# Performance work log

Hardware: AMD Instinct MI355X
Metric: run time of the kernel (lower is better)

Reference implementation:

```python
import jax, jax.numpy as jnp
import numpy as np

K = 128      # classes
CIN = 128    # ch_in
CL = 128     # ch_latent
B, H, W = 8, 1, 8192
SLOPE = 0.01 # F.leaky_relu default
EPS = 1e-5   # BatchNorm eps


def lrelu(x):
    return jnp.where(x >= 0, x, SLOPE * x)


def conv1x1(x, w, b):
    # x: (B,C,H,W), w: (O,C), b: (O,)
    return jnp.einsum('bchw,oc->bohw', x, w) + b[None, :, None, None]


def bn_eval(x, gamma, beta, mean, var):
    scale = gamma * jax.lax.rsqrt(var + EPS)
    return x * scale[None, :, None, None] + (beta - mean * scale)[None, :, None, None]


def setup_inputs() -> dict:
    key = jax.random.key(0)
    ks = jax.random.split(key, 16)
    def w(k, shape, fan_in):
        return jax.random.normal(k, shape, jnp.float32) / np.sqrt(fan_in)
    return {
        'x_in': jax.random.normal(ks[0], (B, CIN, H, W), jnp.float32),
        'cl1_w': w(ks[1], (CL, CIN), CIN), 'cl1_b': jnp.zeros((CL,), jnp.float32),
        'bn1_gamma': jnp.ones((CL,), jnp.float32), 'bn1_beta': jnp.zeros((CL,), jnp.float32),
        'bn1_mean': 0.1 * jax.random.normal(ks[2], (CL,), jnp.float32),
        'bn1_var': jax.random.uniform(ks[3], (CL,), jnp.float32, 0.5, 1.5),
        'cl2_w': w(ks[4], (CL, CL), CL), 'cl2_b': jnp.zeros((CL,), jnp.float32),
        'cl3_w': w(ks[5], (K + 1, CL), CL), 'cl3_b': jnp.zeros((K + 1,), jnp.float32),
        'reg1_w': w(ks[6], (CL, CIN), CIN), 'reg1_b': jnp.zeros((CL,), jnp.float32),
        'bnr_gamma': jnp.ones((CL,), jnp.float32), 'bnr_beta': jnp.zeros((CL,), jnp.float32),
        'bnr_mean': 0.1 * jax.random.normal(ks[7], (CL,), jnp.float32),
        'bnr_var': jax.random.uniform(ks[8], (CL,), jnp.float32, 0.5, 1.5),
        'cm2_w': w(ks[9], (K, CL, 32), CL), 'cm2_b': jnp.zeros((K, 32), jnp.float32),
        'cm3_w': w(ks[10], (K, 32, 1), 32), 'cm3_b': jnp.zeros((K, 1), jnp.float32),
    }


def reference(x_in, cl1_w, cl1_b, bn1_gamma, bn1_beta, bn1_mean, bn1_var,
              cl2_w, cl2_b, cl3_w, cl3_b,
              reg1_w, reg1_b, bnr_gamma, bnr_beta, bnr_mean, bnr_var,
              cm2_w, cm2_b, cm3_w, cm3_b):
    # classification branch
    x = lrelu(bn_eval(conv1x1(x_in, cl1_w, cl1_b), bn1_gamma, bn1_beta, bn1_mean, bn1_var))
    x = lrelu(conv1x1(x, cl2_w, cl2_b))
    x = conv1x1(x, cl3_w, cl3_b)                    # (B, K+1, H, W)
    logits = x[:, :K]
    mask = lrelu(x[:, -1:])                          # (B,1,H,W)
    inds = jnp.argmax(logits, axis=1)                # (B,H,W) int
    inds_r = inds.reshape(-1).astype(jnp.int32)      # (N,)
    xr = lrelu(bn_eval(conv1x1(x_in, reg1_w, reg1_b), bnr_gamma, bnr_beta, bnr_mean, bnr_var))
    # torch: transpose(1,3).reshape(-1, C)  -> (B,W,H,C) flatten
    xr = jnp.transpose(xr, (0, 3, 2, 1)).reshape(-1, CL)   # (N, CL)
    # CondMul 1: per-pixel gathered weight (N,CL,32)
    h = lrelu(jnp.einsum('ni,nio->no', xr, cm2_w[inds_r]) + cm2_b[inds_r])
    # CondMul 2: (N,32)->(N,1)
    reg = jnp.einsum('ni,nio->no', h, cm3_w[inds_r]) + cm3_b[inds_r]
    reg = reg.reshape(B, 1, 1, -1)                   # (B,1,1,H*W)
    x_real = (inds[:, None].astype(jnp.float32) + reg) * (1.0 / K)
    return x_real, mask
```

## Files before the change

kernel.cpp:

```cpp
#include <hip/hip_runtime.h>
#include <math.h>

#define NPOS 65536
#define NCH  128
#define DELTA 0.008f

#define OFF_XR   0u
#define OFF_W1T  8388608u
#define OFF_W2T  (OFF_W1T + 16384u)
#define OFF_W3T  (OFF_W2T + 16384u)
#define OFF_B1F  (OFF_W3T + 16384u)
#define OFF_BRF  (OFF_B1F + 128u)
#define OFF_B2F  (OFF_BRF + 128u)
#define OFF_B3F  (OFF_B2F + 128u)
#define OFF_BF16 (OFF_B3F + 132u)
#define OFF_INT  (OFF_BF16 + 329728u)

#define UW1H 0u
#define UW1L 16384u
#define UWRH 32768u
#define UWRL 49152u
#define UW2H 65536u
#define UW2L 81920u
#define UW3H 98304u
#define UW3L 116736u
#define UW2K 135168u

#define NST 2080

typedef short bf16x8 __attribute__((ext_vector_type(8)));
typedef float f32x4 __attribute__((ext_vector_type(4)));
#define MFMA16 __builtin_amdgcn_mfma_f32_16x16x32_bf16

__device__ __forceinline__ float lrelu(float v) { return v >= 0.0f ? v : 0.01f * v; }
__device__ __forceinline__ unsigned short f2bf(float f) {
    unsigned u = __float_as_uint(f);
    return (unsigned short)((u + 0x7fffu + ((u >> 16) & 1u)) >> 16);
}
__device__ __forceinline__ float bf2f(unsigned short h) {
    return __uint_as_float(((unsigned)h) << 16);
}
__device__ __forceinline__ unsigned long long pack4(unsigned short a, unsigned short b,
                                                    unsigned short c, unsigned short d) {
    return (unsigned long long)a | ((unsigned long long)b << 16)
         | ((unsigned long long)c << 32) | ((unsigned long long)d << 48);
}

__global__ void k_prep(const float* __restrict__ cl1_w, const float* __restrict__ cl1_b,
                       const float* __restrict__ g1, const float* __restrict__ be1,
                       const float* __restrict__ mu1, const float* __restrict__ va1,
                       const float* __restrict__ cl2_w, const float* __restrict__ cl2_b,
                       const float* __restrict__ cl3_w, const float* __restrict__ cl3_b,
                       const float* __restrict__ reg1_w, const float* __restrict__ reg1_b,
                       const float* __restrict__ gr, const float* __restrict__ ber,
                       const float* __restrict__ mur, const float* __restrict__ var_,
                       const float* __restrict__ cm2w,
                       float* __restrict__ ws_f, unsigned short* __restrict__ wbf,
                       int* __restrict__ hist, int* __restrict__ fixcnt)
{
    const int bid = blockIdx.x;
    const int t = threadIdx.x;
    if (bid >= 128) {
        __shared__ float tl[32 * 132];
        int k = bid - 128;
        #pragma unroll
        for (int i = 0; i < 32; ++i) {
            float v = cm2w[(unsigned)k * 4096u + i * 128 + t];
            int ci = i * 4 + (t >> 5), o = t & 31;
            tl[o * 132 + ci] = v;
        }
        __syncthreads();
        #pragma unroll
        for (int i = 0; i < 32; ++i)
            wbf[UW2K + (unsigned)k * 4096u + i * 128 + t] = f2bf(tl[i * 132 + t]);
        return;
    }
    int tid = bid * 128 + t;
    int cin = tid >> 7, cout = tid & 127;
    float s1 = g1[cout] / sqrtf(va1[cout] + 1e-5f);
    float sr = gr[cout] / sqrtf(var_[cout] + 1e-5f);
    float w1 = cl1_w[cout * 128 + cin] * s1;
    float wr = reg1_w[cout * 128 + cin] * sr;
    float w2 = cl2_w[cout * 128 + cin];
    float w3 = cl3_w[cout * 128 + cin];
    ws_f[OFF_W1T + tid] = w1;
    ws_f[OFF_W2T + tid] = w2;
    ws_f[OFF_W3T + tid] = w3;
    int j = cout * 128 + cin;
    unsigned short h;
    h = f2bf(w1); wbf[UW1H + j] = h; wbf[UW1L + j] = f2bf(w1 - bf2f(h));
    h = f2bf(wr); wbf[UWRH + j] = h; wbf[UWRL + j] = f2bf(wr - bf2f(h));
    h = f2bf(w2); wbf[UW2H + j] = h; wbf[UW2L + j] = f2bf(w2 - bf2f(h));
    h = f2bf(w3); wbf[UW3H + j] = h; wbf[UW3L + j] = f2bf(w3 - bf2f(h));
    if (tid < 2048) {
        int r = tid >> 7, ci = tid & 127;
        float v = (r == 0) ? cl3_w[128 * 128 + ci] : 0.0f;
        int jj = (128 + r) * 128 + ci;
        h = f2bf(v); wbf[UW3H + jj] = h; wbf[UW3L + jj] = f2bf(v - bf2f(h));
    }
    if (tid < 128) {
        float s1b = g1[tid] / sqrtf(va1[tid] + 1e-5f);
        float srb = gr[tid] / sqrtf(var_[tid] + 1e-5f);
        ws_f[OFF_B1F + tid] = cl1_b[tid] * s1b + be1[tid] - mu1[tid] * s1b;
        ws_f[OFF_BRF + tid] = reg1_b[tid] * srb + ber[tid] - mur[tid] * srb;
        ws_f[OFF_B2F + tid] = cl2_b[tid];
        hist[tid] = 0;
    }
    if (tid < 129) ws_f[OFF_B3F + tid] = cl3_b[tid];
    if (tid == 0) fixcnt[0] = 0;
}

__global__ __launch_bounds__(256, 2)
void k_fused(const float* __restrict__ X, const float* __restrict__ wsf,
             const unsigned short* __restrict__ wbf,
             float* __restrict__ XR, float* __restrict__ out_mask,
             int* __restrict__ inds, int* __restrict__ fixcnt,
             int* __restrict__ fixlist)
{
    __shared__ __align__(16) unsigned short XBh[64 * 136];
    __shared__ __align__(16) unsigned short XBl[64 * 136];
    __shared__ float sm1[4 * 64];
    __shared__ float sm2[4 * 64];
    __shared__ int   si1[4 * 64];

    const int t = threadIdx.x;
    const int lane = t & 63;
    const int cl16 = lane & 15;
    const int q8 = (lane >> 4) * 8;
    const int q4 = (lane >> 4) * 4;
    const int wv = __builtin_amdgcn_readfirstlane(t >> 6);
    const unsigned nt64 = blockIdx.x * 64u;
    const unsigned base = nt64 + (nt64 >> 13) * 1040384u;

    const unsigned short* W1H = wbf + UW1H; const unsigned short* W1L = wbf + UW1L;
    const unsigned short* WRH = wbf + UWRH; const unsigned short* WRL = wbf + UWRL;
    const unsigned short* W2H = wbf + UW2H; const unsigned short* W2L = wbf + UW2L;
    const unsigned short* W3H = wbf + UW3H; const unsigned short* W3L = wbf + UW3L;
    const float* b1f = wsf + OFF_B1F;
    const float* brf = wsf + OFF_BRF;
    const float* b2f = wsf + OFF_B2F;
    const float* b3f = wsf + OFF_B3F;

    const f32x4 vzero = {0.f, 0.f, 0.f, 0.f};

    {
        const int pos = t & 63, cig = t >> 6;
        #pragma unroll
        for (int l = 0; l < 8; ++l) {
            int ci0 = cig * 32 + l * 4;
            float v0 = X[base + (unsigned)(ci0 + 0) * 8192u + pos];
            float v1 = X[base + (unsigned)(ci0 + 1) * 8192u + pos];
            float v2 = X[base + (unsigned)(ci0 + 2) * 8192u + pos];
            float v3 = X[base + (unsigned)(ci0 + 3) * 8192u + pos];
            unsigned short h0 = f2bf(v0), h1 = f2bf(v1), h2 = f2bf(v2), h3 = f2bf(v3);
            unsigned long long ph = pack4(h0, h1, h2, h3);
            unsigned long long pl = pack4(f2bf(v0 - bf2f(h0)), f2bf(v1 - bf2f(h1)),
                                          f2bf(v2 - bf2f(h2)), f2bf(v3 - bf2f(h3)));
            *(unsigned long long*)&XBh[pos * 136 + ci0] = ph;
            *(unsigned long long*)&XBl[pos * 136 + ci0] = pl;
        }
    }
    __syncthreads();

    f32x4 aY[2][4], aR[2][4];
    #pragma unroll
    for (int m = 0; m < 2; ++m)
        #pragma unroll
        for (int n = 0; n < 4; ++n) { aY[m][n] = vzero; aR[m][n] = vzero; }
    #pragma unroll
    for (int kt = 0; kt < 4; ++kt) {
        bf16x8 Bh[4], Bl[4];
        #pragma unroll
        for (int n = 0; n < 4; ++n) {
            int bo = (n * 16 + cl16) * 136 + kt * 32 + q8;
            Bh[n] = *(const bf16x8*)&XBh[bo];
            Bl[n] = *(const bf16x8*)&XBl[bo];
        }
        #pragma unroll
        for (int m = 0; m < 2; ++m) {
            int ao = (wv * 32 + m * 16 + cl16) * 128 + kt * 32 + q8;
            bf16x8 a1h = *(const bf16x8*)&W1H[ao], a1l = *(const bf16x8*)&W1L[ao];
            bf16x8 arh = *(const bf16x8*)&WRH[ao], arl = *(const bf16x8*)&WRL[ao];
            #pragma unroll
            for (int n = 0; n < 4; ++n) {
                aY[m][n] = MFMA16(a1h, Bl[n], aY[m][n], 0, 0, 0);
                aY[m][n] = MFMA16(a1l, Bh[n], aY[m][n], 0, 0, 0);
                aY[m][n] = MFMA16(a1h, Bh[n], aY[m][n], 0, 0, 0);
                aR[m][n] = MFMA16(arh, Bl[n], aR[m][n], 0, 0, 0);
                aR[m][n] = MFMA16(arl, Bh[n], aR[m][n], 0, 0, 0);
                aR[m][n] = MFMA16(arh, Bh[n], aR[m][n], 0, 0, 0);
            }
        }
    }
    __syncthreads();

    {
        #pragma unroll
        for (int m = 0; m < 2; ++m) {
            int cb = wv * 32 + m * 16 + q4;
            float br0 = brf[cb], br1 = brf[cb + 1], br2 = brf[cb + 2], br3 = brf[cb + 3];
            #pragma unroll
            for (int n = 0; n < 4; ++n) {
                unsigned pb = (nt64 + n * 16 + cl16) * 128u + cb;
                XR[pb]     = lrelu(aR[m][n][0] + br0);
                XR[pb + 1] = lrelu(aR[m][n][1] + br1);
                XR[pb + 2] = lrelu(aR[m][n][2] + br2);
                XR[pb + 3] = lrelu(aR[m][n][3] + br3);
            }
        }
    }
    {
        #pragma unroll
        for (int m = 0; m < 2; ++m) {
            int cb = wv * 32 + m * 16 + q4;
            float b0 = b1f[cb], b1 = b1f[cb + 1], b2 = b1f[cb + 2], b3 = b1f[cb + 3];
            #pragma unroll
            for (int n = 0; n < 4; ++n) {
                float v0 = lrelu(aY[m][n][0] + b0), v1 = lrelu(aY[m][n][1] + b1);
                float v2 = lrelu(aY[m][n][2] + b2), v3 = lrelu(aY[m][n][3] + b3);
                unsigned short h0 = f2bf(v0), h1 = f2bf(v1), h2 = f2bf(v2), h3 = f2bf(v3);
                unsigned long long ph = pack4(h0, h1, h2, h3);
                unsigned long long pl = pack4(f2bf(v0 - bf2f(h0)), f2bf(v1 - bf2f(h1)),
                                              f2bf(v2 - bf2f(h2)), f2bf(v3 - bf2f(h3)));
                int idx = (n * 16 + cl16) * 136 + cb;
                *(unsigned long long*)&XBh[idx] = ph;
                *(unsigned long long*)&XBl[idx] = pl;
            }
        }
    }
    __syncthreads();

    f32x4 aZ[2][4];
    #pragma unroll
    for (int m = 0; m < 2; ++m)
        #pragma unroll
        for (int n = 0; n < 4; ++n) aZ[m][n] = vzero;
    #pragma unroll
    for (int kt = 0; kt < 4; ++kt) {
        bf16x8 Bh[4], Bl[4];
        #pragma unroll
        for (int n = 0; n < 4; ++n) {
            int bo = (n * 16 + cl16) * 136 + kt * 32 + q8;
            Bh[n] = *(const bf16x8*)&XBh[bo];
            Bl[n] = *(const bf16x8*)&XBl[bo];
        }
        #pragma unroll
        for (int m = 0; m < 2; ++m) {
            int ao = (wv * 32 + m * 16 + cl16) * 128 + kt * 32 + q8;
            bf16x8 ah = *(const bf16x8*)&W2H[ao], al = *(const bf16x8*)&W2L[ao];
            #pragma unroll
            for (int n = 0; n < 4; ++n) {
                aZ[m][n] = MFMA16(ah, Bl[n], aZ[m][n], 0, 0, 0);
                aZ[m][n] = MFMA16(al, Bh[n], aZ[m][n], 0, 0, 0);
                aZ[m][n] = MFMA16(ah, Bh[n], aZ[m][n], 0, 0, 0);
            }
        }
    }
    __syncthreads();
    {
        #pragma unroll
        for (int m = 0; m < 2; ++m) {
            int cb = wv * 32 + m * 16 + q4;
            float b0 = b2f[cb], b1 = b2f[cb + 1], b2 = b2f[cb + 2], b3 = b2f[cb + 3];
            #pragma unroll
            for (int n = 0; n < 4; ++n) {
                float v0 = lrelu(aZ[m][n][0] + b0), v1 = lrelu(aZ[m][n][1] + b1);
                float v2 = lrelu(aZ[m][n][2] + b2), v3 = lrelu(aZ[m][n][3] + b3);
                unsigned short h0 = f2bf(v0), h1 = f2bf(v1), h2 = f2bf(v2), h3 = f2bf(v3);
                unsigned long long ph = pack4(h0, h1, h2, h3);
                unsigned long long pl = pack4(f2bf(v0 - bf2f(h0)), f2bf(v1 - bf2f(h1)),
                                              f2bf(v2 - bf2f(h2)), f2bf(v3 - bf2f(h3)));
                int idx = (n * 16 + cl16) * 136 + cb;
                *(unsigned long long*)&XBh[idx] = ph;
                *(unsigned long long*)&XBl[idx] = pl;
            }
        }
    }
    __syncthreads();

    f32x4 aL[2][4], aM[4];
    #pragma unroll
    for (int m = 0; m < 2; ++m)
        #pragma unroll
        for (int n = 0; n < 4; ++n) aL[m][n] = vzero;
    #pragma unroll
    for (int n = 0; n < 4; ++n) aM[n] = vzero;
    #pragma unroll
    for (int kt = 0; kt < 4; ++kt) {
        bf16x8 Bh[4], Bl[4];
        #pragma unroll
        for (int n = 0; n < 4; ++n) {
            int bo = (n * 16 + cl16) * 136 + kt * 32 + q8;
            Bh[n] = *(const bf16x8*)&XBh[bo];
            Bl[n] = *(const bf16x8*)&XBl[bo];
        }
        #pragma unroll
        for (int m = 0; m < 2; ++m) {
            int ao = (wv * 32 + m * 16 + cl16) * 128 + kt * 32 + q8;
            bf16x8 ah = *(const bf16x8*)&W3H[ao], al = *(const bf16x8*)&W3L[ao];
            #pragma unroll
            for (int n = 0; n < 4; ++n) {
                aL[m][n] = MFMA16(ah, Bl[n], aL[m][n], 0, 0, 0);
                aL[m][n] = MFMA16(al, Bh[n], aL[m][n], 0, 0, 0);
                aL[m][n] = MFMA16(ah, Bh[n], aL[m][n], 0, 0, 0);
            }
        }
        if (wv == 3) {
            int ao = (128 + cl16) * 128 + kt * 32 + q8;
            bf16x8 ah = *(const bf16x8*)&W3H[ao], al = *(const bf16x8*)&W3L[ao];
            #pragma unroll
            for (int n = 0; n < 4; ++n) {
                aM[n] = MFMA16(ah, Bl[n], aM[n], 0, 0, 0);
                aM[n] = MFMA16(al, Bh[n], aM[n], 0, 0, 0);
                aM[n] = MFMA16(ah, Bh[n], aM[n], 0, 0, 0);
            }
        }
    }

    {
        float bb[2][4];
        #pragma unroll
        for (int m = 0; m < 2; ++m) {
            int cb = wv * 32 + m * 16 + q4;
            bb[m][0] = b3f[cb]; bb[m][1] = b3f[cb + 1];
            bb[m][2] = b3f[cb + 2]; bb[m][3] = b3f[cb + 3];
        }
        float m1[4], m2[4]; int i1[4];
        #pragma unroll
        for (int n = 0; n < 4; ++n) {
            m1[n] = -1e30f; m2[n] = -1e30f; i1[n] = 0;
            #pragma unroll
            for (int m = 0; m < 2; ++m) {
                int cb = wv * 32 + m * 16 + q4;
                #pragma unroll
                for (int r = 0; r < 4; ++r) {
                    float v = aL[m][n][r] + bb[m][r];
                    if (v > m1[n]) { m2[n] = m1[n]; m1[n] = v; i1[n] = cb + r; }
                    else if (v > m2[n]) m2[n] = v;
                }
            }
        }
        #pragma unroll
        for (int off = 16; off <= 32; off <<= 1) {
            #pragma unroll
            for (int n = 0; n < 4; ++n) {
                float om1 = __shfl_xor(m1[n], off);
                float om2 = __shfl_xor(m2[n], off);
                int   oi1 = __shfl_xor(i1[n], off);
                if (om1 > m1[n] || (om1 == m1[n] && oi1 < i1[n])) {
                    m2[n] = fmaxf(m1[n], om2); m1[n] = om1; i1[n] = oi1;
                } else {
                    m2[n] = fmaxf(m2[n], om1);
                }
            }
        }
        if ((lane >> 4) == 0) {
            #pragma unroll
            for (int n = 0; n < 4; ++n) {
                sm1[wv * 64 + n * 16 + cl16] = m1[n];
                sm2[wv * 64 + n * 16 + cl16] = m2[n];
                si1[wv * 64 + n * 16 + cl16] = i1[n];
            }
        }
    }
    if (wv == 3 && (lane >> 4) == 0) {
        float mb = b3f[128];
        #pragma unroll
        for (int n = 0; n < 4; ++n)
            out_mask[nt64 + n * 16 + cl16] = lrelu(aM[n][0] + mb);
    }
    __syncthreads();
    if (t < 64) {
        float m1 = sm1[t], m2 = sm2[t];
        int i1 = si1[t];
        #pragma unroll
        for (int w = 1; w < 4; ++w) {
            float v1 = sm1[w * 64 + t];
            float v2 = sm2[w * 64 + t];
            int   vi = si1[w * 64 + t];
            if (v1 > m1) { m2 = fmaxf(m1, v2); m1 = v1; i1 = vi; }
            else         { m2 = fmaxf(m2, v1); }
        }
        int n = nt64 + t;
        inds[n] = i1;
        if (m1 - m2 < DELTA) {
            int slot = atomicAdd(fixcnt, 1);
            fixlist[slot] = n;
        }
    }
}

__global__ __launch_bounds__(256, 4)
void k_fix(const float* __restrict__ X, const float* __restrict__ wsf,
           const int* __restrict__ fixcnt, const int* __restrict__ fixlist,
           int* __restrict__ inds)
{
    const int cnt = fixcnt[0];
    const int t = threadIdx.x;
    const int lane = t & 63;
    const int wv = t >> 6;
    const float* W1T = wsf + OFF_W1T;
    const float* W2T = wsf + OFF_W2T;
    const float* W3T = wsf + OFF_W3T;
    const float* b1f = wsf + OFF_B1F;
    const float* b2f = wsf + OFF_B2F;
    const float* b3f = wsf + OFF_B3F;

    for (int idx = blockIdx.x * 4 + wv; idx < cnt; idx += 1024) {
        int n = fixlist[idx];
        const float* xb = X + (unsigned)(n >> 13) * 1048576u + (unsigned)(n & 8191);
        float x0 = xb[(unsigned)lane * 8192u];
        float x1 = xb[(unsigned)(64 + lane) * 8192u];
        float a0, a1;
        a0 = 0.f; a1 = 0.f;
        for (int ci = 0; ci < 64; ++ci) {
            float xv = __shfl(x0, ci);
            const float* wr = W1T + ci * 128;
            a0 = fmaf(wr[lane], xv, a0);
            a1 = fmaf(wr[64 + lane], xv, a1);
        }
        for (int ci = 0; ci < 64; ++ci) {
            float xv = __shfl(x1, ci);
            const float* wr = W1T + (64 + ci) * 128;
            a0 = fmaf(wr[lane], xv, a0);
            a1 = fmaf(wr[64 + lane], xv, a1);
        }
        x0 = lrelu(a0 + b1f[lane]); x1 = lrelu(a1 + b1f[64 + lane]);
        a0 = 0.f; a1 = 0.f;
        for (int ci = 0; ci < 64; ++ci) {
            float xv = __shfl(x0, ci);
            const float* wr = W2T + ci * 128;
            a0 = fmaf(wr[lane], xv, a0);
            a1 = fmaf(wr[64 + lane], xv, a1);
        }
        for (int ci = 0; ci < 64; ++ci) {
            float xv = __shfl(x1, ci);
            const float* wr = W2T + (64 + ci) * 128;
            a0 = fmaf(wr[lane], xv, a0);
            a1 = fmaf(wr[64 + lane], xv, a1);
        }
        x0 = lrelu(a0 + b2f[lane]); x1 = lrelu(a1 + b2f[64 + lane]);
        a0 = 0.f; a1 = 0.f;
        for (int ci = 0; ci < 64; ++ci) {
            float xv = __shfl(x0, ci);
            const float* wr = W3T + ci * 128;
            a0 = fmaf(wr[lane], xv, a0);
            a1 = fmaf(wr[64 + lane], xv, a1);
        }
        for (int ci = 0; ci < 64; ++ci) {
            float xv = __shfl(x1, ci);
            const float* wr = W3T + (64 + ci) * 128;
            a0 = fmaf(wr[lane], xv, a0);
            a1 = fmaf(wr[64 + lane], xv, a1);
        }
        float L0 = a0 + b3f[lane], L1 = a1 + b3f[64 + lane];
        float v; int id;
        if (L0 >= L1) { v = L0; id = lane; } else { v = L1; id = 64 + lane; }
        #pragma unroll
        for (int off = 1; off < 64; off <<= 1) {
            float ov = __shfl_xor(v, off);
            int   oi = __shfl_xor(id, off);
            if (ov > v || (ov == v && oi < id)) { v = ov; id = oi; }
        }
        if (lane == 0) inds[n] = id;
    }
}

__global__ void k_hist(const int* __restrict__ inds, int* __restrict__ hist)
{
    __shared__ int lh[128];
    int t = threadIdx.x;
    if (t < 128) lh[t] = 0;
    __syncthreads();
    atomicAdd(&lh[inds[blockIdx.x * 256 + t]], 1);
    __syncthreads();
    if (t < 128 && lh[t] > 0) atomicAdd(&hist[t], lh[t]);
}

__global__ void k_scan(const int* __restrict__ hist, int* __restrict__ off,
                       int* __restrict__ cur, int* __restrict__ tiles,
                       int* __restrict__ ntt)
{
    __shared__ int s[128];
    __shared__ int s2[128];
    int t = threadIdx.x;
    int v = hist[t];
    int ntk = (v + 127) >> 7;
    s[t] = v;
    s2[t] = ntk;
    __syncthreads();
    for (int d = 1; d < 128; d <<= 1) {
        int a  = (t >= d) ? s[t - d]  : 0;
        int a2 = (t >= d) ? s2[t - d] : 0;
        __syncthreads();
        s[t] += a;
        s2[t] += a2;
        __syncthreads();
    }
    off[t] = s[t] - v;
    cur[t] = s[t] - v;
    int tb = s2[t] - ntk;
    for (int j = 0; j < ntk; ++j)
        tiles[tb + j] = (t << 16) | j;
    if (t == 127) ntt[0] = s2[127];
}

__global__ void k_scatter(const int* __restrict__ inds, int* __restrict__ cur,
                          int* __restrict__ bucket)
{
    __shared__ int lh[128];
    __shared__ int gb[128];
    int t = threadIdx.x;
    if (t < 128) lh[t] = 0;
    __syncthreads();
    int n = blockIdx.x * 256 + t;
    int id = inds[n];
    int r = atomicAdd(&lh[id], 1);
    __syncthreads();
    if (t < 128 && lh[t] > 0) gb[t] = atomicAdd(&cur[t], lh[t]);
    __syncthreads();
    bucket[gb[id] + r] = n;
}

__global__ __launch_bounds__(256, 4)
void k_reg(const float* __restrict__ XR, const unsigned short* __restrict__ wbf,
           const float* __restrict__ cm2b, const float* __restrict__ cm3w,
           const float* __restrict__ cm3b, const int* __restrict__ hist,
           const int* __restrict__ off, const int* __restrict__ bucket,
           const int* __restrict__ tiles, const int* __restrict__ ntt,
           float* __restrict__ out)
{
    __shared__ __align__(16) unsigned short XP[8 * NST];
    __shared__ float red[128];
    int bid = blockIdx.x;
    if (bid >= ntt[0]) return;
    int desc = tiles[bid];
    int k = desc >> 16;
    int start = (desc & 0xffff) << 7;
    int cnt = hist[k];
    int base = off[k];
    int t = threadIdx.x;
    int lane = t & 63;
    int wv = __builtin_amdgcn_readfirstlane(t >> 6);
    const int n16 = lane & 15;
    const int quad = lane >> 4;

    #pragma unroll
    for (int half = 0; half < 2; ++half) {
        int rs = (t >> 2) + half * 64;
        int q = t & 3;
        int sidx = start + rs;
        if (sidx >= cnt) sidx = cnt - 1;
        int n = bucket[base + sidx];
        const float4* src = (const float4*)(XR + (unsigned)n * 128u + q * 32);
        unsigned db = (rs >> 4) * NST + q * 512 + (rs & 15) * 8;
        #pragma unroll
        for (int qg = 0; qg < 4; ++qg) {
            float4 fa = src[qg * 2], fb = src[qg * 2 + 1];
            unsigned long long pa = pack4(f2bf(fa.x), f2bf(fa.y), f2bf(fa.z), f2bf(fa.w));
            unsigned long long pb = pack4(f2bf(fb.x), f2bf(fb.y), f2bf(fb.z), f2bf(fb.w));
            *(unsigned long long*)&XP[db + qg * 128]     = pa;
            *(unsigned long long*)&XP[db + qg * 128 + 4] = pb;
        }
    }
    __syncthreads();

    const unsigned short* wb = wbf + UW2K + (unsigned)k * 4096u;
    bf16x8 Bf[2][4];
    #pragma unroll
    for (int nf = 0; nf < 2; ++nf)
        #pragma unroll
        for (int kt = 0; kt < 4; ++kt)
            Bf[nf][kt] = *(const bf16x8*)&wb[(nf * 16 + n16) * 128 + kt * 32 + quad * 8];

    const f32x4 vzero = {0.f, 0.f, 0.f, 0.f};
    f32x4 acc[2][2];
    acc[0][0] = vzero; acc[0][1] = vzero; acc[1][0] = vzero; acc[1][1] = vzero;
    #pragma unroll
    for (int kt = 0; kt < 4; ++kt) {
        bf16x8 Af[2];
        #pragma unroll
        for (int mf = 0; mf < 2; ++mf)
            Af[mf] = *(const bf16x8*)&XP[(wv * 2 + mf) * NST + kt * 512 + lane * 8];
        #pragma unroll
        for (int mf = 0; mf < 2; ++mf)
            #pragma unroll
            for (int nf = 0; nf < 2; ++nf)
                acc[mf][nf] = MFMA16(Af[mf], Bf[nf][kt], acc[mf][nf], 0, 0, 0);
    }

    float b2a = cm2b[k * 32 + n16], b2b = cm2b[k * 32 + 16 + n16];
    float w3a = cm3w[k * 32 + n16], w3b = cm3w[k * 32 + 16 + n16];
    const int m0 = wv * 32;
    #pragma unroll
    for (int mf = 0; mf < 2; ++mf) {
        #pragma unroll
        for (int r = 0; r < 4; ++r) {
            float p = lrelu(acc[mf][0][r] + b2a) * w3a
                    + lrelu(acc[mf][1][r] + b2b) * w3b;
            p += __shfl_xor(p, 1);
            p += __shfl_xor(p, 2);
            p += __shfl_xor(p, 4);
            p += __shfl_xor(p, 8);
            if (n16 == 0)
                red[m0 + mf * 16 + quad * 4 + r] = p;
        }
    }
    __syncthreads();
    if (t < 128 && start + t < cnt) {
        int n2 = bucket[base + start + t];
        out[n2] = ((float)k + red[t] + cm3b[k]) * (1.0f / 128.0f);
    }
}

extern "C" void kernel_launch(void* const* d_in, const int* in_sizes, int n_in,
                              void* d_out, int out_size, void* d_ws, size_t ws_size,
                              hipStream_t stream)
{
    (void)in_sizes; (void)n_in; (void)out_size; (void)ws_size;
    const float* x_in   = (const float*)d_in[0];
    const float* cl1_w  = (const float*)d_in[1];
    const float* cl1_b  = (const float*)d_in[2];
    const float* g1     = (const float*)d_in[3];
    const float* be1    = (const float*)d_in[4];
    const float* mu1    = (const float*)d_in[5];
    const float* va1    = (const float*)d_in[6];
    const float* cl2_w  = (const float*)d_in[7];
    const float* cl2_b  = (const float*)d_in[8];
    const float* cl3_w  = (const float*)d_in[9];
    const float* cl3_b  = (const float*)d_in[10];
    const float* reg1_w = (const float*)d_in[11];
    const float* reg1_b = (const float*)d_in[12];
    const float* gr     = (const float*)d_in[13];
    const float* ber    = (const float*)d_in[14];
    const float* mur    = (const float*)d_in[15];
    const float* var_   = (const float*)d_in[16];
    const float* cm2w   = (const float*)d_in[17];
    const float* cm2b   = (const float*)d_in[18];
    const float* cm3w   = (const float*)d_in[19];
    const float* cm3b   = (const float*)d_in[20];

    float* ws_f = (float*)d_ws;
    float* XR   = ws_f + OFF_XR;
    unsigned short* wbf = (unsigned short*)(ws_f + OFF_BF16);
    int*   wsi    = (int*)(ws_f + OFF_INT);
    int*   inds   = wsi;
    int*   hist   = inds + 65536;
    int*   offb   = hist + 128;
    int*   cur    = offb + 128;
    int*   ntt    = cur + 128;
    int*   fixcnt = ntt + 4;
    int*   tiles  = fixcnt + 4;
    int*   fixlist= tiles + 1024;
    int*   bucket = fixlist + 65536;
    float* out = (float*)d_out;

    hipLaunchKernelGGL(k_prep, dim3(256), dim3(128), 0, stream,
                       cl1_w, cl1_b, g1, be1, mu1, va1, cl2_w, cl2_b, cl3_w, cl3_b,
                       reg1_w, reg1_b, gr, ber, mur, var_, cm2w, ws_f, wbf, hist, fixcnt);
    hipLaunchKernelGGL(k_fused, dim3(1024), dim3(256), 0, stream,
                       x_in, ws_f, wbf, XR, out + 65536, inds, fixcnt, fixlist);
    hipLaunchKernelGGL(k_fix, dim3(256), dim3(256), 0, stream,
                       x_in, ws_f, fixcnt, fixlist, inds);
    hipLaunchKernelGGL(k_hist, dim3(256), dim3(256), 0, stream, inds, hist);
    hipLaunchKernelGGL(k_scan, dim3(1), dim3(128), 0, stream,
                       hist, offb, cur, tiles, ntt);
    hipLaunchKernelGGL(k_scatter, dim3(256), dim3(256), 0, stream, inds, cur, bucket);
    hipLaunchKernelGGL(k_reg, dim3(768), dim3(256), 0, stream,
                       XR, wbf, cm2b, cm3w, cm3b, hist, offb, bucket, tiles, ntt, out);
}
```

Baseline: 244.7 us.

## Store regression latent as bf16, fold histogram into fused kernel, halve reg tiles

```diff
diff --git a/kernel.cpp b/kernel.cpp
--- a/kernel.cpp
+++ b/kernel.cpp
@@ -113,9 +113,9 @@
 __global__ __launch_bounds__(256, 2)
 void k_fused(const float* __restrict__ X, const float* __restrict__ wsf,
              const unsigned short* __restrict__ wbf,
-             float* __restrict__ XR, float* __restrict__ out_mask,
-             int* __restrict__ inds, int* __restrict__ fixcnt,
-             int* __restrict__ fixlist)
+             unsigned short* __restrict__ XRB, float* __restrict__ out_mask,
+             int* __restrict__ inds, int* __restrict__ hist,
+             int* __restrict__ fixcnt, int* __restrict__ fixlist)
 {
     __shared__ __align__(16) unsigned short XBh[64 * 136];
     __shared__ __align__(16) unsigned short XBl[64 * 136];
@@ -202,10 +202,12 @@
             #pragma unroll
             for (int n = 0; n < 4; ++n) {
                 unsigned pb = (nt64 + n * 16 + cl16) * 128u + cb;
-                XR[pb]     = lrelu(aR[m][n][0] + br0);
-                XR[pb + 1] = lrelu(aR[m][n][1] + br1);
-                XR[pb + 2] = lrelu(aR[m][n][2] + br2);
-                XR[pb + 3] = lrelu(aR[m][n][3] + br3);
+                ushort4 xo;
+                xo.x = f2bf(lrelu(aR[m][n][0] + br0));
+                xo.y = f2bf(lrelu(aR[m][n][1] + br1));
+                xo.z = f2bf(lrelu(aR[m][n][2] + br2));
+                xo.w = f2bf(lrelu(aR[m][n][3] + br3));
+                *(ushort4*)&XRB[pb] = xo;
             }
         }
     }
@@ -383,6 +385,7 @@
         }
         int n = nt64 + t;
         inds[n] = i1;
+        atomicAdd(&hist[i1], 1);
         if (m1 - m2 < DELTA) {
             int slot = atomicAdd(fixcnt, 1);
             fixlist[slot] = n;
@@ -393,7 +396,7 @@
 __global__ __launch_bounds__(256, 4)
 void k_fix(const float* __restrict__ X, const float* __restrict__ wsf,
            const int* __restrict__ fixcnt, const int* __restrict__ fixlist,
-           int* __restrict__ inds)
+           int* __restrict__ inds, int* __restrict__ hist)
 {
     const int cnt = fixcnt[0];
     const int t = threadIdx.x;
@@ -462,19 +465,15 @@
             int   oi = __shfl_xor(id, off);
             if (ov > v || (ov == v && oi < id)) { v = ov; id = oi; }
         }
-        if (lane == 0) inds[n] = id;
-    }
-}
-
-__global__ void k_hist(const int* __restrict__ inds, int* __restrict__ hist)
-{
-    __shared__ int lh[128];
-    int t = threadIdx.x;
-    if (t < 128) lh[t] = 0;
-    __syncthreads();
-    atomicAdd(&lh[inds[blockIdx.x * 256 + t]], 1);
-    __syncthreads();
-    if (t < 128 && lh[t] > 0) atomicAdd(&hist[t], lh[t]);
+        if (lane == 0) {
+            int old = inds[n];
+            if (id != old) {
+                inds[n] = id;
+                atomicAdd(&hist[id], 1);
+                atomicSub(&hist[old], 1);
+            }
+        }
+    }
 }
 
 __global__ void k_scan(const int* __restrict__ hist, int* __restrict__ off,
@@ -485,7 +484,7 @@
     __shared__ int s2[128];
     int t = threadIdx.x;
     int v = hist[t];
-    int ntk = (v + 127) >> 7;
+    int ntk = (v + 63) >> 6;
     s[t] = v;
     s2[t] = ntk;
     __syncthreads();
@@ -523,20 +522,20 @@
 }
 
 __global__ __launch_bounds__(256, 4)
-void k_reg(const float* __restrict__ XR, const unsigned short* __restrict__ wbf,
+void k_reg(const unsigned short* __restrict__ XRB, const unsigned short* __restrict__ wbf,
            const float* __restrict__ cm2b, const float* __restrict__ cm3w,
            const float* __restrict__ cm3b, const int* __restrict__ hist,
            const int* __restrict__ off, const int* __restrict__ bucket,
            const int* __restrict__ tiles, const int* __restrict__ ntt,
            float* __restrict__ out)
 {
-    __shared__ __align__(16) unsigned short XP[8 * NST];
-    __shared__ float red[128];
+    __shared__ __align__(16) unsigned short XP[4 * NST];
+    __shared__ float red[64];
     int bid = blockIdx.x;
     if (bid >= ntt[0]) return;
     int desc = tiles[bid];
     int k = desc >> 16;
-    int start = (desc & 0xffff) << 7;
+    int start = (desc & 0xffff) << 6;
     int cnt = hist[k];
     int base = off[k];
     int t = threadIdx.x;
@@ -545,23 +544,19 @@
     const int n16 = lane & 15;
     const int quad = lane >> 4;
 
-    #pragma unroll
-    for (int half = 0; half < 2; ++half) {
-        int rs = (t >> 2) + half * 64;
+    {
+        int rs = t >> 2;
         int q = t & 3;
         int sidx = start + rs;
         if (sidx >= cnt) sidx = cnt - 1;
         int n = bucket[base + sidx];
-        const float4* src = (const float4*)(XR + (unsigned)n * 128u + q * 32);
+        const uint4* src = (const uint4*)(XRB + (unsigned)n * 128u + q * 32);
+        uint4 a0 = src[0], a1 = src[1], a2 = src[2], a3 = src[3];
         unsigned db = (rs >> 4) * NST + q * 512 + (rs & 15) * 8;
-        #pragma unroll
-        for (int qg = 0; qg < 4; ++qg) {
-            float4 fa = src[qg * 2], fb = src[qg * 2 + 1];
-            unsigned long long pa = pack4(f2bf(fa.x), f2bf(fa.y), f2bf(fa.z), f2bf(fa.w));
-            unsigned long long pb = pack4(f2bf(fb.x), f2bf(fb.y), f2bf(fb.z), f2bf(fb.w));
-            *(unsigned long long*)&XP[db + qg * 128]     = pa;
-            *(unsigned long long*)&XP[db + qg * 128 + 4] = pb;
-        }
+        *(uint4*)&XP[db]       = a0;
+        *(uint4*)&XP[db + 128] = a1;
+        *(uint4*)&XP[db + 256] = a2;
+        *(uint4*)&XP[db + 384] = a3;
     }
     __syncthreads();
 
@@ -574,40 +569,31 @@
             Bf[nf][kt] = *(const bf16x8*)&wb[(nf * 16 + n16) * 128 + kt * 32 + quad * 8];
 
     const f32x4 vzero = {0.f, 0.f, 0.f, 0.f};
-    f32x4 acc[2][2];
-    acc[0][0] = vzero; acc[0][1] = vzero; acc[1][0] = vzero; acc[1][1] = vzero;
+    f32x4 acc[2];
+    acc[0] = vzero; acc[1] = vzero;
     #pragma unroll
     for (int kt = 0; kt < 4; ++kt) {
-        bf16x8 Af[2];
-        #pragma unroll
-        for (int mf = 0; mf < 2; ++mf)
-            Af[mf] = *(const bf16x8*)&XP[(wv * 2 + mf) * NST + kt * 512 + lane * 8];
-        #pragma unroll
-        for (int mf = 0; mf < 2; ++mf)
-            #pragma unroll
-            for (int nf = 0; nf < 2; ++nf)
-                acc[mf][nf] = MFMA16(Af[mf], Bf[nf][kt], acc[mf][nf], 0, 0, 0);
+        bf16x8 Af = *(const bf16x8*)&XP[wv * NST + kt * 512 + lane * 8];
+        #pragma unroll
+        for (int nf = 0; nf < 2; ++nf)
+            acc[nf] = MFMA16(Af, Bf[nf][kt], acc[nf], 0, 0, 0);
     }
 
     float b2a = cm2b[k * 32 + n16], b2b = cm2b[k * 32 + 16 + n16];
     float w3a = cm3w[k * 32 + n16], w3b = cm3w[k * 32 + 16 + n16];
-    const int m0 = wv * 32;
-    #pragma unroll
-    for (int mf = 0; mf < 2; ++mf) {
-        #pragma unroll
-        for (int r = 0; r < 4; ++r) {
-            float p = lrelu(acc[mf][0][r] + b2a) * w3a
-                    + lrelu(acc[mf][1][r] + b2b) * w3b;
-            p += __shfl_xor(p, 1);
-            p += __shfl_xor(p, 2);
-            p += __shfl_xor(p, 4);
-            p += __shfl_xor(p, 8);
-            if (n16 == 0)
-                red[m0 + mf * 16 + quad * 4 + r] = p;
-        }
-    }
-    __syncthreads();
-    if (t < 128 && start + t < cnt) {
+    #pragma unroll
+    for (int r = 0; r < 4; ++r) {
+        float p = lrelu(acc[0][r] + b2a) * w3a
+                + lrelu(acc[1][r] + b2b) * w3b;
+        p += __shfl_xor(p, 1);
+        p += __shfl_xor(p, 2);
+        p += __shfl_xor(p, 4);
+        p += __shfl_xor(p, 8);
+        if (n16 == 0)
+            red[wv * 16 + quad * 4 + r] = p;
+    }
+    __syncthreads();
+    if (t < 64 && start + t < cnt) {
         int n2 = bucket[base + start + t];
         out[n2] = ((float)k + red[t] + cm3b[k]) * (1.0f / 128.0f);
     }
@@ -641,7 +627,7 @@
     const float* cm3b   = (const float*)d_in[20];
 
     float* ws_f = (float*)d_ws;
-    float* XR   = ws_f + OFF_XR;
+    unsigned short* XRB = (unsigned short*)(ws_f + OFF_XR);
     unsigned short* wbf = (unsigned short*)(ws_f + OFF_BF16);
     int*   wsi    = (int*)(ws_f + OFF_INT);
     int*   inds   = wsi;
@@ -651,7 +637,7 @@
     int*   ntt    = cur + 128;
     int*   fixcnt = ntt + 4;
     int*   tiles  = fixcnt + 4;
-    int*   fixlist= tiles + 1024;
+    int*   fixlist= tiles + 1536;
     int*   bucket = fixlist + 65536;
     float* out = (float*)d_out;
 
@@ -659,13 +645,12 @@
                        cl1_w, cl1_b, g1, be1, mu1, va1, cl2_w, cl2_b, cl3_w, cl3_b,
                        reg1_w, reg1_b, gr, ber, mur, var_, cm2w, ws_f, wbf, hist, fixcnt);
     hipLaunchKernelGGL(k_fused, dim3(1024), dim3(256), 0, stream,
-                       x_in, ws_f, wbf, XR, out + 65536, inds, fixcnt, fixlist);
+                       x_in, ws_f, wbf, XRB, out + 65536, inds, hist, fixcnt, fixlist);
     hipLaunchKernelGGL(k_fix, dim3(256), dim3(256), 0, stream,
-                       x_in, ws_f, fixcnt, fixlist, inds);
-    hipLaunchKernelGGL(k_hist, dim3(256), dim3(256), 0, stream, inds, hist);
+                       x_in, ws_f, fixcnt, fixlist, inds, hist);
     hipLaunchKernelGGL(k_scan, dim3(1), dim3(128), 0, stream,
                        hist, offb, cur, tiles, ntt);
     hipLaunchKernelGGL(k_scatter, dim3(256), dim3(256), 0, stream, inds, cur, bucket);
-    hipLaunchKernelGGL(k_reg, dim3(768), dim3(256), 0, stream,
-                       XR, wbf, cm2b, cm3w, cm3b, hist, offb, bucket, tiles, ntt, out);
-}
+    hipLaunchKernelGGL(k_reg, dim3(1536), dim3(256), 0, stream,
+                       XRB, wbf, cm2b, cm3w, cm3b, hist, offb, bucket, tiles, ntt, out);
+}
```

Result: slower. 325.2 us (+32.9%).
